# Optimization experiments

Hardware: AMD Instinct MI355X
Metric: run time of the kernel (lower is better)

The kernel has to match this reference:

```python
import jax, jax.numpy as jnp
import numpy as np

EPS = 1e-7
B, N, DIM, NH, HD, WIN, HASH_WIN = 2, 1024, 512, 8, 64, 64, 8


def expmap0(v, c):
    sqrt_c = jnp.clip(jnp.sqrt(c), EPS)
    v_norm = jnp.linalg.norm(v, axis=-1, keepdims=True)
    is_zero = v_norm < EPS
    safe = jnp.clip(v_norm, EPS)
    mag = jnp.tanh(sqrt_c * safe) / sqrt_c
    return jnp.where(is_zero, jnp.zeros_like(v), mag * (v / safe))


def poincare_dist(x, y, c):
    # x: (B,H,N,1,D), y: (B,H,N,W,D), c: (B,1,1,1,1) -> (B,H,N,W)
    sqrt_c = jnp.clip(jnp.sqrt(c), EPS)
    x2 = jnp.sum(x * x, -1, keepdims=True)
    y2 = jnp.sum(y * y, -1, keepdims=True)
    xy = jnp.sum(x * y, -1, keepdims=True)
    num = (1 - 2 * c * xy + c * y2) * x + (1 - c * x2) * (-y)
    den = 1 - 2 * c * xy + c * c * x2 * y2
    diff = num / jnp.clip(den, EPS)
    dn = jnp.linalg.norm(diff, axis=-1)
    arg = jnp.minimum(jnp.squeeze(sqrt_c, -1) * jnp.clip(dn, EPS), 1.0 - EPS)
    return 2.0 * jnp.arctanh(arg) / jnp.squeeze(sqrt_c, -1)


def sliding_windows(t, w):
    # t: (B,H,N,D) -> (B,H,N,w,D), left-padded causal window
    Bb, H, Nn, D = t.shape
    pad = jnp.zeros((Bb, H, w - 1, D), t.dtype)
    tp = jnp.concatenate([pad, t], axis=2)
    idx = jnp.arange(w)[None, :] + jnp.arange(Nn)[:, None]  # (N,w)
    return tp[:, :, idx, :]


def layernorm(x, s, b):
    m = jnp.mean(x, -1, keepdims=True)
    v = jnp.var(x, -1, keepdims=True)
    return (x - m) / jnp.sqrt(v + 1e-6) * s + b


def rope(x, cos, sin):
    # x: (B,N,H,hd), cos/sin: (N, hd//2) -- complex rotation in real arithmetic
    xr, xi = jnp.split(x, 2, axis=-1)
    cos = cos[None, :, None, :]
    sin = sin[None, :, None, :]
    return jnp.concatenate([xr * cos - xi * sin, xr * sin + xi * cos], axis=-1)


def setup_inputs() -> dict:
    key = jax.random.key(0)
    ks = jax.random.split(key, 10)
    x = jax.random.normal(ks[0], (B, N, DIM), jnp.float32)
    pos = jnp.arange(N, dtype=jnp.float32)
    inv = 1.0 / (10000.0 ** (jnp.arange(0, HD, 2, dtype=jnp.float32) / HD))
    ang = pos[:, None] * inv[None, :]  # (N, HD//2)
    freqs_cos, freqs_sin = jnp.cos(ang), jnp.sin(ang)
    c = jax.random.uniform(ks[1], (B,), jnp.float32) * 0.9 + 0.1
    s = 0.02
    Wq = jax.random.normal(ks[2], (DIM, DIM), jnp.float32) * s
    Wk = jax.random.normal(ks[3], (DIM, DIM), jnp.float32) * s
    Wv = jax.random.normal(ks[4], (DIM, DIM), jnp.float32) * s
    Wo = jax.random.normal(ks[5], (DIM, DIM), jnp.float32) * s
    W1 = jax.random.normal(ks[6], (DIM, 4 * DIM), jnp.float32) * s
    W2 = jax.random.normal(ks[7], (4 * DIM, DIM), jnp.float32) * s
    bq = jnp.zeros((DIM,)); bk = jnp.zeros((DIM,)); bv = jnp.zeros((DIM,))
    bo = jnp.zeros((DIM,)); b1 = jnp.zeros((4 * DIM,)); b2 = jnp.zeros((DIM,))
    ln1_s = jnp.ones((DIM,)); ln1_b = jnp.zeros((DIM,))
    ln2_s = jnp.ones((DIM,)); ln2_b = jnp.zeros((DIM,))
    geo_scale = jnp.ones((NH, 1, 1), jnp.float32)
    hash_offset = jax.random.normal(ks[8], (1, 1, NH, HD), jnp.float32) * 0.01
    return dict(x=x, freqs_cos=freqs_cos, freqs_sin=freqs_sin, c=c,
                Wq=Wq, bq=bq, Wk=Wk, bk=bk, Wv=Wv, bv=bv, Wo=Wo, bo=bo,
                W1=W1, b1=b1, W2=W2, b2=b2,
                ln1_s=ln1_s, ln1_b=ln1_b, ln2_s=ln2_s, ln2_b=ln2_b,
                geo_scale=geo_scale, hash_offset=hash_offset)


def reference(x, freqs_cos, freqs_sin, c, Wq, bq, Wk, bk, Wv, bv, Wo, bo,
              W1, b1, W2, b2, ln1_s, ln1_b, ln2_s, ln2_b, geo_scale, hash_offset):
    x_res = x
    xn = layernorm(x, ln1_s, ln1_b)
    q = (xn @ Wq + bq).reshape(B, N, NH, HD)
    k = (xn @ Wk + bk).reshape(B, N, NH, HD)
    v = (xn @ Wv + bv).reshape(B, N, NH, HD)
    q = q + hash_offset * jnp.log(1.0 + HASH_WIN)
    q_rot = rope(q, freqs_cos, freqs_sin)
    k_rot = rope(k, freqs_cos, freqs_sin)
    c_b = c.reshape(B, 1, 1, 1)
    q_h = expmap0(q_rot, c_b)
    k_h = expmap0(k_rot, c_b)
    q_h, k_h, v = (t.transpose(0, 2, 1, 3) for t in (q_h, k_h, v))  # (B,H,N,D)
    k_win = sliding_windows(k_h, WIN)  # (B,H,N,W,D)
    v_win = sliding_windows(v, WIN)
    dist = poincare_dist(q_h[:, :, :, None, :], k_win, c.reshape(B, 1, 1, 1, 1))  # (B,H,N,W)
    scores = -geo_scale * dist
    w = jax.nn.softmax(scores, axis=-1)
    attn = jnp.einsum('bhnw,bhnwd->bhnd', w, v_win)
    attn = attn.transpose(0, 2, 1, 3).reshape(B, N, DIM)
    x_out = x_res + (attn @ Wo + bo)
    h = layernorm(x_out, ln2_s, ln2_b)
    ffn = jax.nn.gelu(h @ W1 + b1) @ W2 + b2
    return x_out + ffn
```

## Files before the change

kernel.cpp:

```cpp
#include <hip/hip_runtime.h>
#include <math.h>
#include <stdint.h>

#define Bn   2
#define Nn   1024
#define DIMn 512
#define NHn  8
#define HDn  64
#define QKVS 1536
#define EPSF 1e-7f

typedef __attribute__((ext_vector_type(8))) short short8;
typedef __attribute__((ext_vector_type(4))) float floatx4;

__device__ __forceinline__ unsigned short f2bf(float f) {
  union { float f; uint32_t u; } v; v.f = f;
  uint32_t u = v.u;
  return (unsigned short)((u + 0x7FFFu + ((u >> 16) & 1u)) >> 16);
}
__device__ __forceinline__ float bf2f(unsigned short h) {
  union { uint32_t u; float f; } v; v.u = ((uint32_t)h) << 16;
  return v.f;
}

__device__ __forceinline__ float wsum(float v) {
#pragma unroll
  for (int m = 32; m >= 1; m >>= 1) v += __shfl_xor(v, m, 64);
  return v;
}
__device__ __forceinline__ float wmax(float v) {
#pragma unroll
  for (int m = 32; m >= 1; m >>= 1) v = fmaxf(v, __shfl_xor(v, m, 64));
  return v;
}

__device__ __forceinline__ float gelu_tanh(float x) {
  const float k0 = 0.7978845608028654f;
  float x3 = x * x * x;
  return 0.5f * x * (1.f + tanhf(k0 * (x + 0.044715f * x3)));
}

__device__ __forceinline__ void glds16(const unsigned short* g, unsigned short* l) {
  __builtin_amdgcn_global_load_lds((const __attribute__((address_space(1))) void*)g,
                                   (__attribute__((address_space(3))) void*)l, 16, 0, 0);
}

__global__ __launch_bounds__(256) void prep_kernel(
    const float* __restrict__ Wq, const float* __restrict__ Wk,
    const float* __restrict__ Wv, const float* __restrict__ Wo,
    const float* __restrict__ W1, const float* __restrict__ W2,
    unsigned short* __restrict__ Wcat_hi, unsigned short* __restrict__ Wcat_lo,
    unsigned short* __restrict__ Wo_t, unsigned short* __restrict__ W1_t,
    unsigned short* __restrict__ W2_t,
    const float* __restrict__ bq, const float* __restrict__ bk,
    const float* __restrict__ bv, float* __restrict__ bias_cat,
    const float* __restrict__ x, const float* __restrict__ ln1s,
    const float* __restrict__ ln1b,
    unsigned short* __restrict__ xn_hi, unsigned short* __restrict__ xn_lo) {
  __shared__ float t[32][33];
  __shared__ float red[2][4];
  int bid = blockIdx.x;
  int tid = threadIdx.x;
  if (bid == 3072) {
    for (int i = tid; i < 512; i += 256) {
      bias_cat[i] = bq[i];
      bias_cat[512 + i] = bk[i];
      bias_cat[1024 + i] = bv[i];
    }
    return;
  }
  if (bid > 3072) {
    int row = bid - 3073;
    const float* xr = x + (size_t)row * DIMn;
    float2 xv = *(const float2*)(xr + tid * 2);
    float s  = xv.x + xv.y;
    float s2 = xv.x * xv.x + xv.y * xv.y;
    s = wsum(s); s2 = wsum(s2);
    int wv = tid >> 6;
    if ((tid & 63) == 0) { red[0][wv] = s; red[1][wv] = s2; }
    __syncthreads();
    s  = red[0][0] + red[0][1] + red[0][2] + red[0][3];
    s2 = red[1][0] + red[1][1] + red[1][2] + red[1][3];
    float mean = s * (1.f / DIMn);
    float var  = s2 * (1.f / DIMn) - mean * mean;
    float rstd = rsqrtf(var + 1e-6f);
    int d = tid * 2;
    float2 gv = *(const float2*)(ln1s + d);
    float2 bv2 = *(const float2*)(ln1b + d);
    float o0 = (xv.x - mean) * rstd * gv.x + bv2.x;
    float o1 = (xv.y - mean) * rstd * gv.y + bv2.y;
    size_t idx = (size_t)row * DIMn + d;
    unsigned short h0 = f2bf(o0), h1 = f2bf(o1);
    ushort2 hv; hv.x = h0; hv.y = h1;
    *(ushort2*)(xn_hi + idx) = hv;
    ushort2 lv; lv.x = f2bf(o0 - bf2f(h0)); lv.y = f2bf(o1 - bf2f(h1));
    *(ushort2*)(xn_lo + idx) = lv;
    return;
  }
  const float* W;
  unsigned short* hi;
  unsigned short* lo = nullptr;
  int K, N, tix;
  if (bid < 256)       { W = Wq; hi = Wcat_hi;               lo = Wcat_lo;               K = 512;  N = 512;  tix = bid; }
  else if (bid < 512)  { W = Wk; hi = Wcat_hi + 512 * 512;   lo = Wcat_lo + 512 * 512;   K = 512;  N = 512;  tix = bid - 256; }
  else if (bid < 768)  { W = Wv; hi = Wcat_hi + 1024 * 512;  K = 512;  N = 512;  tix = bid - 512; }
  else if (bid < 1024) { W = Wo; hi = Wo_t;                  K = 512;  N = 512;  tix = bid - 768; }
  else if (bid < 2048) { W = W1; hi = W1_t;                  K = 512;  N = 2048; tix = bid - 1024; }
  else                 { W = W2; hi = W2_t;                  K = 2048; N = 512;  tix = bid - 2048; }
  int ntn = N >> 5;
  int kt = tix / ntn, nt = tix - kt * ntn;
  int k0 = kt * 32, n0 = nt * 32;
  for (int i = tid; i < 1024; i += 256) {
    int r = i >> 5, c = i & 31;
    t[r][c] = W[(size_t)(k0 + r) * N + n0 + c];
  }
  __syncthreads();
  for (int i = tid; i < 1024; i += 256) {
    int r = i >> 5, c = i & 31;
    float v = t[c][r];
    unsigned short h = f2bf(v);
    size_t oi = (size_t)(n0 + r) * K + k0 + c;
    hi[oi] = h;
    if (lo) lo[oi] = f2bf(v - bf2f(h));
  }
}

__global__ __launch_bounds__(256) void ln_kernel(const float* __restrict__ x,
                                                 const float* __restrict__ g,
                                                 const float* __restrict__ be,
                                                 unsigned short* __restrict__ yhi) {
  __shared__ float red[2][4];
  int row = blockIdx.x;
  int tid = threadIdx.x;
  const float* xr = x + (size_t)row * DIMn;
  float2 xv = *(const float2*)(xr + tid * 2);
  float s  = xv.x + xv.y;
  float s2 = xv.x * xv.x + xv.y * xv.y;
  s = wsum(s); s2 = wsum(s2);
  int wv = tid >> 6;
  if ((tid & 63) == 0) { red[0][wv] = s; red[1][wv] = s2; }
  __syncthreads();
  s  = red[0][0] + red[0][1] + red[0][2] + red[0][3];
  s2 = red[1][0] + red[1][1] + red[1][2] + red[1][3];
  float mean = s * (1.f / DIMn);
  float var  = s2 * (1.f / DIMn) - mean * mean;
  float rstd = rsqrtf(var + 1e-6f);
  int d = tid * 2;
  float2 gv = *(const float2*)(g + d);
  float2 bv = *(const float2*)(be + d);
  float o0 = (xv.x - mean) * rstd * gv.x + bv.x;
  float o1 = (xv.y - mean) * rstd * gv.y + bv.y;
  size_t idx = (size_t)row * DIMn + d;
  ushort2 hv; hv.x = f2bf(o0); hv.y = f2bf(o1);
  *(ushort2*)(yhi + idx) = hv;
}

template <int BM, int BN, int BKT, int SPLIT, int EPI, int OUTBF16>
__global__ __launch_bounds__(256) void gemm_mfma(
    const unsigned short* __restrict__ Ahi, const unsigned short* __restrict__ Alo,
    const unsigned short* __restrict__ Bhi, const unsigned short* __restrict__ Blo,
    const float* __restrict__ bias, const float* __restrict__ res,
    void* __restrict__ outp, int M, int N, int K) {
  constexpr int FI = BM / 32, FJ = BN / 32;
  constexpr int AE = BM * BKT, BE = BN * BKT;
  constexpr int NB = (SPLIT > 0) ? 2 : 1;
  constexpr int CPR = BKT / 8;
  constexpr int ACH = BM * CPR, BCH = BN * CPR;
  __shared__ unsigned short smem[NB * (AE + BE)];
  unsigned short* AsHi = smem;
  unsigned short* AsLo = smem + ((SPLIT > 0) ? AE : 0);
  unsigned short* BsHi = smem + NB * AE;
  unsigned short* BsLo = BsHi + ((SPLIT > 0) ? BE : 0);

  int tid = threadIdx.x;
  int lane = tid & 63;
  int wid = tid >> 6;
  int wm = (wid >> 1) * (BM / 2), wn = (wid & 1) * (BN / 2);
  int bm = blockIdx.y * BM, bn = blockIdx.x * BN;
  int m16 = lane & 15, kg = lane >> 4;
  bool dos = (SPLIT == 1) || (SPLIT == 2 && bn < 1024);

  floatx4 acc[FI][FJ];
#pragma unroll
  for (int i = 0; i < FI; ++i)
#pragma unroll
    for (int j = 0; j < FJ; ++j) { floatx4 z = {0.f, 0.f, 0.f, 0.f}; acc[i][j] = z; }

  const unsigned short* aph = Ahi + (size_t)bm * K;
  const unsigned short* bph = Bhi + (size_t)bn * K;
  const unsigned short* apl = (SPLIT > 0) ? (Alo + (size_t)bm * K) : nullptr;
  const unsigned short* bpl = (SPLIT > 0) ? (Blo + (size_t)bn * K) : nullptr;

  for (int k0 = 0; k0 < K; k0 += BKT) {
#pragma unroll
    for (int c = tid; c < ACH; c += 256) {
      int row = c / CPR, kk = (c % CPR) * 8;
      glds16(aph + (size_t)row * K + k0 + kk, AsHi + c * 8);
      if (SPLIT > 0 && dos) glds16(apl + (size_t)row * K + k0 + kk, AsLo + c * 8);
    }
#pragma unroll
    for (int c = tid; c < BCH; c += 256) {
      int row = c / CPR, kk = (c % CPR) * 8;
      glds16(bph + (size_t)row * K + k0 + kk, BsHi + c * 8);
      if (SPLIT > 0 && dos) glds16(bpl + (size_t)row * K + k0 + kk, BsLo + c * 8);
    }
    __syncthreads();

#pragma unroll
    for (int ks = 0; ks < BKT / 32; ++ks) {
      short8 ah[FI], bh[FJ];
      short8 al[(SPLIT > 0) ? FI : 1], bl[(SPLIT > 0) ? FJ : 1];
#pragma unroll
      for (int i = 0; i < FI; ++i) {
        int r = wm + i * 16 + m16;
        ah[i] = *(const short8*)&AsHi[r * BKT + ks * 32 + kg * 8];
        if (SPLIT > 0 && dos) al[i] = *(const short8*)&AsLo[r * BKT + ks * 32 + kg * 8];
      }
#pragma unroll
      for (int j = 0; j < FJ; ++j) {
        int r = wn + j * 16 + m16;
        bh[j] = *(const short8*)&BsHi[r * BKT + ks * 32 + kg * 8];
        if (SPLIT > 0 && dos) bl[j] = *(const short8*)&BsLo[r * BKT + ks * 32 + kg * 8];
      }
#pragma unroll
      for (int i = 0; i < FI; ++i)
#pragma unroll
        for (int j = 0; j < FJ; ++j) {
          acc[i][j] = __builtin_amdgcn_mfma_f32_16x16x32_bf16(ah[i], bh[j], acc[i][j], 0, 0, 0);
          if (SPLIT > 0) {
            if (dos) {
              acc[i][j] = __builtin_amdgcn_mfma_f32_16x16x32_bf16(al[i], bh[j], acc[i][j], 0, 0, 0);
              acc[i][j] = __builtin_amdgcn_mfma_f32_16x16x32_bf16(ah[i], bl[j], acc[i][j], 0, 0, 0);
            }
          }
        }
    }
    __syncthreads();
  }

#pragma unroll
  for (int i = 0; i < FI; ++i) {
    int gr0 = bm + wm + i * 16 + kg * 4;
#pragma unroll
    for (int j = 0; j < FJ; ++j) {
      int gc = bn + wn + j * 16 + m16;
      float bsv = bias[gc];
#pragma unroll
      for (int r = 0; r < 4; ++r) {
        size_t idx = (size_t)(gr0 + r) * N + gc;
        float v = acc[i][j][r] + bsv;
        if constexpr (EPI == 1) v += res[idx];
        if constexpr (EPI == 2) v = gelu_tanh(v);
        if constexpr (OUTBF16) ((unsigned short*)outp)[idx] = f2bf(v);
        else ((float*)outp)[idx] = v;
      }
    }
  }
}

__global__ __launch_bounds__(512) void attn_fused(const float* __restrict__ qkv,
                                                  const float* __restrict__ fcos,
                                                  const float* __restrict__ fsin,
                                                  const float* __restrict__ cvec,
                                                  const float* __restrict__ geo,
                                                  const float* __restrict__ hash,
                                                  unsigned short* __restrict__ attn_out) {
  __shared__ unsigned short Qhi[32][72], Qlo[32][72];
  __shared__ unsigned short Khi[96][72], Klo[96][72];
  __shared__ unsigned short Vt[64][104];
  __shared__ unsigned short Pb[32][104];
  __shared__ float Sf[32][97];
  __shared__ float x2s[32], bxs[32], y2s[96], gys[96];

  int tid = threadIdx.x, lane = tid & 63, wv = tid >> 6;
  int bid = blockIdx.x;
  int nt = bid & 31, h = (bid >> 5) & 7, b = bid >> 8;
  int n0 = nt * 32;
  float c = cvec[b];
  float sqc = sqrtf(c);
  float rsqc = 1.f / sqc;
  float gs = geo[h];
  int dr = lane & 31;
  bool hih = lane >= 32;
  const float LOG9 = 2.1972245773362196f;
  float hofr = hash[h * HDn + dr] * LOG9;
  float hofi = hash[h * HDn + dr + 32] * LOG9;

  for (int i = tid; i < 32 * 52; i += 512) ((uint32_t*)Pb)[i] = 0u;

#pragma unroll
  for (int i = 0; i < 4; ++i) {
    int q = wv * 4 + i;
    int n = n0 + q;
    size_t bas = (size_t)(b * Nn + n) * QKVS + h * HDn;
    float qr = qkv[bas + dr] + hofr;
    float qi = qkv[bas + dr + 32] + hofi;
    float cs = fcos[n * 32 + dr], sn = fsin[n * 32 + dr];
    float qv = hih ? (qr * sn + qi * cs) : (qr * cs - qi * sn);
    float nq = sqrtf(wsum(qv * qv));
    float sq = fmaxf(nq, EPSF);
    float t = sqc * sq;
    float em = expf(-2.f * t);
    float opem = 1.f + em;
    float mag = ((1.f - em) / opem) * rsqc;
    float sech2 = 4.f * em / (opem * opem);
    float oq = (nq < EPSF) ? 0.f : mag * (qv / sq);
    unsigned short hh = f2bf(oq);
    Qhi[q][lane] = hh;
    Qlo[q][lane] = f2bf(oq - bf2f(hh));
    if (lane == 0) {
      x2s[q] = (nq < EPSF) ? 0.f : mag * mag;
      bxs[q] = (nq < EPSF) ? 1.f : sech2;
    }
  }
#pragma unroll 4
  for (int i = 0; i < 12; ++i) {
    int r = wv * 12 + i;
    int gi = n0 - 64 + r;
    float ok = 0.f, vf = 0.f, y2 = 0.f, gy = 1.f;
    if (gi >= 0) {
      size_t bas = (size_t)(b * Nn + gi) * QKVS + h * HDn;
      float kr = qkv[bas + 512 + dr];
      float ki = qkv[bas + 512 + dr + 32];
      vf = qkv[bas + 1024 + lane];
      float cs = fcos[gi * 32 + dr], sn = fsin[gi * 32 + dr];
      float kv = hih ? (kr * sn + ki * cs) : (kr * cs - ki * sn);
      float nk = sqrtf(wsum(kv * kv));
      float sk = fmaxf(nk, EPSF);
      float t = sqc * sk;
      float em = expf(-2.f * t);
      float opem = 1.f + em;
      float mag = ((1.f - em) / opem) * rsqc;
      float sech2 = 4.f * em / (opem * opem);
      ok = (nk < EPSF) ? 0.f : mag * (kv / sk);
      y2 = (nk < EPSF) ? 0.f : mag * mag;
      gy = (nk < EPSF) ? 1.f : sech2;
    }
    unsigned short hh = f2bf(ok);
    Khi[r][lane] = hh;
    Klo[r][lane] = f2bf(ok - bf2f(hh));
    Vt[lane][r] = f2bf(vf);
    if (lane == 0) { y2s[r] = y2; gys[r] = gy; }
  }
  __syncthreads();

  int m16 = lane & 15, kg = lane >> 4;
#pragma unroll
  for (int uu = 0; uu < 2; ++uu) {
    int u = wv + uu * 8;
    if (u < 12) {
      int mt = u / 6, ntile = u % 6;
      floatx4 acc = {0.f, 0.f, 0.f, 0.f};
#pragma unroll
      for (int ks = 0; ks < 2; ++ks) {
        short8 ah = *(const short8*)&Qhi[mt * 16 + m16][ks * 32 + kg * 8];
        short8 al = *(const short8*)&Qlo[mt * 16 + m16][ks * 32 + kg * 8];
        short8 bh = *(const short8*)&Khi[ntile * 16 + m16][ks * 32 + kg * 8];
        short8 bl = *(const short8*)&Klo[ntile * 16 + m16][ks * 32 + kg * 8];
        acc = __builtin_amdgcn_mfma_f32_16x16x32_bf16(ah, bh, acc, 0, 0, 0);
        acc = __builtin_amdgcn_mfma_f32_16x16x32_bf16(al, bh, acc, 0, 0, 0);
        acc = __builtin_amdgcn_mfma_f32_16x16x32_bf16(ah, bl, acc, 0, 0, 0);
      }
#pragma unroll
      for (int r = 0; r < 4; ++r) Sf[mt * 16 + kg * 4 + r][ntile * 16 + m16] = acc[r];
    }
  }
  __syncthreads();

#pragma unroll
  for (int i = 0; i < 4; ++i) {
    int nl = wv * 4 + i;
    int r = nl + 1 + lane;
    float xy = Sf[nl][r];
    float x2 = x2s[nl], y2 = y2s[r];
    float bx = bxs[nl], gy = gys[r];

    float den = fmaf(c * c * x2, y2, fmaf(-2.f * c, xy, 1.f));
    den = fmaxf(den, EPSF);
    float rden = 1.f / den;
    float s2 = fmaxf(x2 - 2.f * xy + y2, 0.f);
    float z = sqrtf(c * s2 * rden);
    float omz2 = bx * gy * rden;
    float opz = 1.f + fminf(z, 1.f);
    float ratio = fminf(opz * opz / omz2, 1.9999999e7f);
    float sc = -gs * logf(ratio) * rsqc;

    float mx = wmax(sc);
    float e = expf(sc - mx);
    float se = wsum(e);
    Pb[nl][r] = f2bf(e / se);
  }
  __syncthreads();

  {
    int mt = wv >> 2, ntile = wv & 3;
    floatx4 acc = {0.f, 0.f, 0.f, 0.f};
#pragma unroll
    for (int ks = 0; ks < 3; ++ks) {
      short8 a = *(const short8*)&Pb[mt * 16 + m16][ks * 32 + kg * 8];
      short8 bb = *(const short8*)&Vt[ntile * 16 + m16][ks * 32 + kg * 8];
      acc = __builtin_amdgcn_mfma_f32_16x16x32_bf16(a, bb, acc, 0, 0, 0);
    }
#pragma unroll
    for (int r = 0; r < 4; ++r) {
      int qrow = mt * 16 + kg * 4 + r;
      int d = ntile * 16 + m16;
      attn_out[(size_t)(b * Nn + n0 + qrow) * DIMn + h * HDn + d] = f2bf(acc[r]);
    }
  }
}

extern "C" void kernel_launch(void* const* d_in, const int* in_sizes, int n_in,
                              void* d_out, int out_size, void* d_ws, size_t ws_size,
                              hipStream_t stream) {
  const float* x    = (const float*)d_in[0];
  const float* fcos = (const float*)d_in[1];
  const float* fsin = (const float*)d_in[2];
  const float* cvec = (const float*)d_in[3];
  const float* Wq = (const float*)d_in[4];  const float* bq = (const float*)d_in[5];
  const float* Wk = (const float*)d_in[6];  const float* bk = (const float*)d_in[7];
  const float* Wv = (const float*)d_in[8];  const float* bv = (const float*)d_in[9];
  const float* Wo = (const float*)d_in[10]; const float* bo = (const float*)d_in[11];
  const float* W1 = (const float*)d_in[12]; const float* b1 = (const float*)d_in[13];
  const float* W2 = (const float*)d_in[14]; const float* b2 = (const float*)d_in[15];
  const float* ln1s = (const float*)d_in[16]; const float* ln1b = (const float*)d_in[17];
  const float* ln2s = (const float*)d_in[18]; const float* ln2b = (const float*)d_in[19];
  const float* geo  = (const float*)d_in[20]; const float* hash = (const float*)d_in[21];
  float* out = (float*)d_out;
  char* base = (char*)d_ws;

  unsigned short* Wcat_hi = (unsigned short*)(base + 0);
  unsigned short* Wcat_lo = (unsigned short*)(base + 1572864);
  unsigned short* Wo_t    = (unsigned short*)(base + 3145728);
  unsigned short* W1_t    = (unsigned short*)(base + 3670016);
  unsigned short* W2_t    = (unsigned short*)(base + 5767168);
  unsigned short* xn_hi   = (unsigned short*)(base + 7864320);
  unsigned short* xn_lo   = (unsigned short*)(base + 9961472);
  float*          qkv     = (float*)(base + 12058624);
  unsigned short* attnb   = (unsigned short*)(base + 7864320);
  float*          xout    = (float*)(base + 9961472);
  unsigned short* hbuf    = (unsigned short*)(base + 14155776);
  unsigned short* mid     = (unsigned short*)(base + 16252928);
  float*          bias_cat= (float*)(base + 24641536);

  const int M = Bn * Nn;

  prep_kernel<<<3073 + M, 256, 0, stream>>>(Wq, Wk, Wv, Wo, W1, W2, Wcat_hi, Wcat_lo,
                                            Wo_t, W1_t, W2_t, bq, bk, bv, bias_cat,
                                            x, ln1s, ln1b, xn_hi, xn_lo);
  gemm_mfma<64, 64, 32, 2, 0, 0><<<dim3(QKVS / 64, M / 64), 256, 0, stream>>>(
      xn_hi, xn_lo, Wcat_hi, Wcat_lo, bias_cat, nullptr, qkv, M, QKVS, 512);
  attn_fused<<<Bn * NHn * (Nn / 32), 512, 0, stream>>>(qkv, fcos, fsin, cvec, geo, hash, attnb);
  gemm_mfma<32, 64, 64, 0, 1, 0><<<dim3(DIMn / 64, M / 32), 256, 0, stream>>>(
      attnb, nullptr, Wo_t, nullptr, bo, x, xout, M, DIMn, 512);
  ln_kernel<<<M, 256, 0, stream>>>(xout, ln2s, ln2b, hbuf);
  gemm_mfma<64, 128, 64, 0, 2, 1><<<dim3(2048 / 128, M / 64), 256, 0, stream>>>(
      hbuf, nullptr, W1_t, nullptr, b1, nullptr, mid, M, 2048, 512);
  gemm_mfma<32, 64, 64, 0, 1, 0><<<dim3(DIMn / 64, M / 32), 256, 0, stream>>>(
      mid, nullptr, W2_t, nullptr, b2, xout, out, M, DIMn, 2048);
}
```

Measured before the change: 193.5 us.

## Vectorize GEMM epilogue via LDS staging, widen QKV K-tile, drop softmax max

The GEMM epilogue now writes the accumulators to shared memory and then emits coalesced float4 loads and stores for bias, residual and output. The prep transpose load is vectorized to float4. The QKV GEMM K-tile grows from 32 to 64. The softmax drops its max-reduction and relies on the scores being non-positive, which saves shuffles but risks underflow if the scores are very negative.

```diff
diff --git a/kernel.cpp b/kernel.cpp
--- a/kernel.cpp
+++ b/kernel.cpp
@@ -12,6 +12,8 @@
 
 typedef __attribute__((ext_vector_type(8))) short short8;
 typedef __attribute__((ext_vector_type(4))) float floatx4;
+typedef __attribute__((ext_vector_type(4))) float fx4;
+typedef __attribute__((ext_vector_type(4))) unsigned short usx4;
 
 __device__ __forceinline__ unsigned short f2bf(float f) {
   union { float f; uint32_t u; } v; v.f = f;
@@ -26,11 +28,6 @@
 __device__ __forceinline__ float wsum(float v) {
 #pragma unroll
   for (int m = 32; m >= 1; m >>= 1) v += __shfl_xor(v, m, 64);
-  return v;
-}
-__device__ __forceinline__ float wmax(float v) {
-#pragma unroll
-  for (int m = 32; m >= 1; m >>= 1) v = fmaxf(v, __shfl_xor(v, m, 64));
   return v;
 }
 
@@ -110,9 +107,10 @@
   int ntn = N >> 5;
   int kt = tix / ntn, nt = tix - kt * ntn;
   int k0 = kt * 32, n0 = nt * 32;
-  for (int i = tid; i < 1024; i += 256) {
-    int r = i >> 5, c = i & 31;
-    t[r][c] = W[(size_t)(k0 + r) * N + n0 + c];
+  {
+    int r = tid >> 3, c = (tid & 7) << 2;
+    fx4 v = *(const fx4*)&W[(size_t)(k0 + r) * N + n0 + c];
+    t[r][c] = v.x; t[r][c + 1] = v.y; t[r][c + 2] = v.z; t[r][c + 3] = v.w;
   }
   __syncthreads();
   for (int i = tid; i < 1024; i += 256) {
@@ -166,7 +164,11 @@
   constexpr int NB = (SPLIT > 0) ? 2 : 1;
   constexpr int CPR = BKT / 8;
   constexpr int ACH = BM * CPR, BCH = BN * CPR;
-  __shared__ unsigned short smem[NB * (AE + BE)];
+  constexpr int CST = BN + 4;
+  constexpr int SMEM_STAGE = NB * (AE + BE);
+  constexpr int SMEM_EPI   = BM * CST * 2;
+  constexpr int SMEM_N = (SMEM_STAGE > SMEM_EPI) ? SMEM_STAGE : SMEM_EPI;
+  __shared__ __align__(16) unsigned short smem[SMEM_N];
   unsigned short* AsHi = smem;
   unsigned short* AsLo = smem + ((SPLIT > 0) ? AE : 0);
   unsigned short* BsHi = smem + NB * AE;
@@ -238,22 +240,37 @@
     __syncthreads();
   }
 
-#pragma unroll
-  for (int i = 0; i < FI; ++i) {
-    int gr0 = bm + wm + i * 16 + kg * 4;
-#pragma unroll
-    for (int j = 0; j < FJ; ++j) {
-      int gc = bn + wn + j * 16 + m16;
-      float bsv = bias[gc];
-#pragma unroll
-      for (int r = 0; r < 4; ++r) {
-        size_t idx = (size_t)(gr0 + r) * N + gc;
-        float v = acc[i][j][r] + bsv;
-        if constexpr (EPI == 1) v += res[idx];
-        if constexpr (EPI == 2) v = gelu_tanh(v);
-        if constexpr (OUTBF16) ((unsigned short*)outp)[idx] = f2bf(v);
-        else ((float*)outp)[idx] = v;
-      }
+  float* Cs = (float*)smem;
+#pragma unroll
+  for (int i = 0; i < FI; ++i)
+#pragma unroll
+    for (int j = 0; j < FJ; ++j)
+#pragma unroll
+      for (int r = 0; r < 4; ++r)
+        Cs[(wm + i * 16 + kg * 4 + r) * CST + wn + j * 16 + m16] = acc[i][j][r];
+  __syncthreads();
+  constexpr int TOT = BM * BN / 4;
+  for (int t = tid; t < TOT; t += 256) {
+    int row = (t << 2) / BN;
+    int col = (t << 2) & (BN - 1);
+    fx4 v = *(const fx4*)&Cs[row * CST + col];
+    fx4 bs = *(const fx4*)&bias[bn + col];
+    v = v + bs;
+    size_t gidx = (size_t)(bm + row) * N + bn + col;
+    if constexpr (EPI == 1) {
+      fx4 rr = *(const fx4*)&res[gidx];
+      v = v + rr;
+    }
+    if constexpr (EPI == 2) {
+      v.x = gelu_tanh(v.x); v.y = gelu_tanh(v.y);
+      v.z = gelu_tanh(v.z); v.w = gelu_tanh(v.w);
+    }
+    if constexpr (OUTBF16) {
+      usx4 h;
+      h.x = f2bf(v.x); h.y = f2bf(v.y); h.z = f2bf(v.z); h.w = f2bf(v.w);
+      *(usx4*)((unsigned short*)outp + gidx) = h;
+    } else {
+      *(fx4*)((float*)outp + gidx) = v;
     }
   }
 }
@@ -385,8 +402,7 @@
     float ratio = fminf(opz * opz / omz2, 1.9999999e7f);
     float sc = -gs * logf(ratio) * rsqc;
 
-    float mx = wmax(sc);
-    float e = expf(sc - mx);
+    float e = expf(sc);
     float se = wsum(e);
     Pb[nl][r] = f2bf(e / se);
   }
@@ -448,7 +464,7 @@
   prep_kernel<<<3073 + M, 256, 0, stream>>>(Wq, Wk, Wv, Wo, W1, W2, Wcat_hi, Wcat_lo,
                                             Wo_t, W1_t, W2_t, bq, bk, bv, bias_cat,
                                             x, ln1s, ln1b, xn_hi, xn_lo);
-  gemm_mfma<64, 64, 32, 2, 0, 0><<<dim3(QKVS / 64, M / 64), 256, 0, stream>>>(
+  gemm_mfma<64, 64, 64, 2, 0, 0><<<dim3(QKVS / 64, M / 64), 256, 0, stream>>>(
       xn_hi, xn_lo, Wcat_hi, Wcat_lo, bias_cat, nullptr, qkv, M, QKVS, 512);
   attn_fused<<<Bn * NHn * (Nn / 32), 512, 0, stream>>>(qkv, fcos, fsin, cvec, geo, hash, attnb);
   gemm_mfma<32, 64, 64, 0, 1, 0><<<dim3(DIMn / 64, M / 32), 256, 0, stream>>>(
```

After: 191.3 us. Within noise of the previous version (-1.1%).
